# Kernel tuning notes

Hardware: AMD Instinct MI355X
Metric: run time of the kernel (lower is better)

Reference implementation:

```python
import jax, jax.numpy as jnp
import numpy as np

B, V, NB, K = 4, 5023, 10, 9
# (Cin, Cout) per NLayer: encoder Linear(3->16) then 3 encoder NLayers, 3 decoder NLayers, Linear(3->3)
CH = [(16, 16), (16, 16), (16, 32), (32, 16), (16, 16), (16, 3)]


def _glorot(key, shape):
    fan_in, fan_out = shape[0], shape[-1]
    s = np.float32(np.sqrt(2.0 / (fan_in + fan_out)))
    return (jax.random.normal(key, shape, dtype=jnp.float32) * s)


def setup_inputs():
    key = jax.random.key(0)
    ks = jax.random.split(key, 4 + 4 * len(CH))
    inp = {}
    inp["x"] = jax.random.normal(ks[0], (B, V, 3), dtype=jnp.float32)
    inp["adj"] = jax.random.randint(ks[1], (V, NB), 0, V + 1, dtype=jnp.int32)
    inp["Win"] = _glorot(ks[2], (3, CH[0][0]))
    inp["Wout"] = _glorot(ks[3], (CH[-1][1], 3))
    for i, (cin, cout) in enumerate(CH):
        k0, k1, k2, k3 = ks[4 + 4 * i], ks[5 + 4 * i], ks[6 + 4 * i], ks[7 + 4 * i]
        inp[f"W{i}"] = _glorot(k0, (cin, K, cout))
        inp[f"b{i}"] = jax.random.normal(k1, (cout,), dtype=jnp.float32) * 0.01
        inp[f"u{i}"] = _glorot(k2, (cin, K))
        inp[f"c{i}"] = jax.random.normal(k3, (K,), dtype=jnp.float32) * 0.01
    return inp


def _pad_gather(t, adj):
    # t: [B, V, ...]; pad a zero row at vertex index 0, gather neighbor features.
    z = jnp.zeros(t.shape[:1] + (1,) + t.shape[2:], t.dtype)
    return jnp.take(jnp.concatenate([z, t], axis=1), adj, axis=1)  # [B, V, NB, ...]


def _nlayer(h, adj, recip, W, b, u, c):
    # h: [B, V, Cin], W: [Cin, K, Cout], u: [Cin, K]
    wx = jnp.einsum('bvc,cko->bvko', h, W)          # [B, V, K, Cout]
    nb_w = _pad_gather(wx, adj)                      # [B, V, NB, K, Cout]
    ux = jnp.einsum('bvc,ck->bvk', h, u)             # [B, V, K]  (u and v maps share self.u)
    nb_u = _pad_gather(ux, adj)                      # [B, V, NB, K]
    q = jax.nn.softmax(ux[:, :, None, :] + nb_u + c, axis=-1)  # softmax over kernel dim
    out = jnp.einsum('bvnk,bvnko->bvo', q, nb_w)     # sum over neighbors & kernels
    return out * recip[None, :, None] + b


def reference(x, adj, Win, Wout, W0, b0, u0, c0, W1, b1, u1, c1, W2, b2, u2, c2,
              W3, b3, u3, c3, W4, b4, u4, c4, W5, b5, u5, c5):
    cnt = jnp.sum(adj != 0, axis=-1).astype(jnp.float32)        # [V]
    recip = jnp.where(cnt > 0, 1.0 / jnp.maximum(cnt, 1.0), 0.0)
    h = jax.nn.relu(x @ Win)
    layers = [(W0, b0, u0, c0), (W1, b1, u1, c1), (W2, b2, u2, c2),
              (W3, b3, u3, c3), (W4, b4, u4, c4), (W5, b5, u5, c5)]
    for (W, b, u, c) in layers:
        h = jax.nn.relu(_nlayer(h, adj, recip, W, b, u, c))
    return h @ Wout
```

## Files before the change

### kernel.cpp

```cpp
#include <hip/hip_runtime.h>

#define NBK 10
#define KK  9

constexpr int Bv  = 4;
constexpr int Vv  = 5023;
constexpr int TOT = Bv * Vv;
constexpr int UXP = 12;

__device__ __forceinline__ float merge16(float* a, int t)
{
#pragma unroll
    for (int j = 0; j < 8; j++) {
        float send = (t & 8) ? a[j] : a[j + 8];
        float keep = (t & 8) ? a[j + 8] : a[j];
        a[j] = keep + __shfl_xor(send, 8, 16);
    }
#pragma unroll
    for (int j = 0; j < 4; j++) {
        float send = (t & 4) ? a[j] : a[j + 4];
        float keep = (t & 4) ? a[j + 4] : a[j];
        a[j] = keep + __shfl_xor(send, 4, 16);
    }
#pragma unroll
    for (int j = 0; j < 2; j++) {
        float send = (t & 2) ? a[j] : a[j + 2];
        float keep = (t & 2) ? a[j + 2] : a[j];
        a[j] = keep + __shfl_xor(send, 2, 16);
    }
    {
        float send = (t & 1) ? a[0] : a[1];
        float keep = (t & 1) ? a[1] : a[0];
        a[0] = keep + __shfl_xor(send, 1, 16);
    }
    return a[0];
}

__global__ __launch_bounds__(256) void enc_l0_kernel(
    const float* __restrict__ x,
    const int*   __restrict__ adj,
    const float* __restrict__ Win,
    const float* __restrict__ u0,
    const float* __restrict__ W,
    const float* __restrict__ bvec,
    const float* __restrict__ cvec,
    const float* __restrict__ unx,
    float* __restrict__ hout,
    float* __restrict__ uxout)
{
    const int tid = threadIdx.x;
    const int g = tid >> 4;
    const int t = tid & 15;
    const int vv = blockIdx.x * 16 + g;
    if (vv >= TOT) return;
    const int b = vv / Vv;
    const int v = vv - b * Vv;
    const float* xB = x + (size_t)b * Vv * 3;

    int nb[NBK];
    const int2* arow = reinterpret_cast<const int2*>(&adj[v * NBK]);
#pragma unroll
    for (int j = 0; j < 5; j++) { int2 p = arow[j]; nb[2 * j] = p.x; nb[2 * j + 1] = p.y; }
    int cnt = 0;
#pragma unroll
    for (int n = 0; n < NBK; n++) cnt += (nb[n] != 0) ? 1 : 0;
    const float rec = cnt ? (1.0f / (float)cnt) : 0.0f;

    const float w0 = Win[t], w1 = Win[16 + t], w2 = Win[32 + t];
    float hn0[NBK];
#pragma unroll
    for (int n = 0; n < NBK; n++) {
        const int a = nb[n];
        float x0 = 0.f, x1 = 0.f, x2 = 0.f;
        if (a) {
            const float* xr = &xB[(size_t)(a - 1) * 3];
            x0 = xr[0]; x1 = xr[1]; x2 = xr[2];
        }
        hn0[n] = fmaxf(x0 * w0 + x1 * w1 + x2 * w2, 0.0f);
    }

    float q[KK] = {};
    if (t < NBK) {
        const float* xo = &xB[(size_t)v * 3];
        const float xo0 = xo[0], xo1 = xo[1], xo2 = xo[2];
        const int a = nb[t];
        float xn0 = 0.f, xn1 = 0.f, xn2 = 0.f;
        if (a) {
            const float* xr = &xB[(size_t)(a - 1) * 3];
            xn0 = xr[0]; xn1 = xr[1]; xn2 = xr[2];
        }
        float hs[16];
#pragma unroll
        for (int c = 0; c < 16; c++) {
            const float ho = fmaxf(xo0 * Win[c] + xo1 * Win[16 + c] + xo2 * Win[32 + c], 0.0f);
            const float hn = fmaxf(xn0 * Win[c] + xn1 * Win[16 + c] + xn2 * Win[32 + c], 0.0f);
            hs[c] = ho + hn;
        }
        float lg[KK];
#pragma unroll
        for (int k = 0; k < KK; k++) {
            float s = cvec[k];
#pragma unroll
            for (int c = 0; c < 16; c++) s = fmaf(hs[c], u0[c * KK + k], s);
            lg[k] = s;
        }
        float m = lg[0];
#pragma unroll
        for (int k = 1; k < KK; k++) m = fmaxf(m, lg[k]);
        float sum = 0.0f;
#pragma unroll
        for (int k = 0; k < KK; k++) { q[k] = __expf(lg[k] - m); sum += q[k]; }
        const float r = 1.0f / sum;
#pragma unroll
        for (int k = 0; k < KK; k++) q[k] *= r;
    }

    float g0[KK];
#pragma unroll
    for (int k = 0; k < KK; k++) g0[k] = 0.0f;
#pragma unroll
    for (int n = 0; n < NBK; n++) {
#pragma unroll
        for (int k = 0; k < KK; k++) {
            const float qnk = __shfl(q[k], n, 16);
            g0[k] = fmaf(qnk, hn0[n], g0[k]);
        }
    }

    float acc[16] = {};
#pragma unroll
    for (int k = 0; k < KK; k++) {
        const float4* wr = reinterpret_cast<const float4*>(&W[((size_t)t * KK + k) * 16]);
#pragma unroll
        for (int o4 = 0; o4 < 4; o4++) {
            const float4 w = wr[o4];
            acc[4 * o4 + 0] = fmaf(g0[k], w.x, acc[4 * o4 + 0]);
            acc[4 * o4 + 1] = fmaf(g0[k], w.y, acc[4 * o4 + 1]);
            acc[4 * o4 + 2] = fmaf(g0[k], w.z, acc[4 * o4 + 2]);
            acc[4 * o4 + 3] = fmaf(g0[k], w.w, acc[4 * o4 + 3]);
        }
    }

    const float o0 = merge16(acc, t);
    const float h0v = fmaxf(fmaf(o0, rec, bvec[t]), 0.0f);
    hout[(size_t)vv * 16 + t] = h0v;

    float uxv = 0.0f;
#pragma unroll
    for (int o = 0; o < 16; o++) {
        const float hb = __shfl(h0v, o, 16);
        if (t < KK) uxv = fmaf(hb, unx[o * KK + t], uxv);
    }
    if (t < KK) uxout[(size_t)vv * UXP + t] = uxv;
}

template<int CIN, int COUT, bool LAST>
__global__ __launch_bounds__(256) void nlayer_kernel(
    const float* __restrict__ hin,
    const float* __restrict__ uxin,
    const int*   __restrict__ adj,
    const float* __restrict__ W,
    const float* __restrict__ bvec,
    const float* __restrict__ cvec,
    const float* __restrict__ unx,
    float* __restrict__ hout,
    float* __restrict__ uxout,
    float* __restrict__ dout)
{
    constexpr int COUTP = (COUT == 32) ? 36 : ((COUT == 16) ? 20 : 4);

    __shared__ __align__(16) float s_w[KK * CIN * COUTP];
    __shared__ __align__(16) float s_q[16][NBK][12];

    const int tid = threadIdx.x;

    for (int i = tid; i < CIN * KK * COUT; i += 256) {
        const int c   = i / (KK * COUT);
        const int rem = i - c * (KK * COUT);
        const int k   = rem / COUT;
        const int o   = rem - k * COUT;
        s_w[(k * CIN + c) * COUTP + o] = W[i];
    }
    __syncthreads();

    const int g = tid >> 4;
    const int t = tid & 15;
    const int vv = blockIdx.x * 16 + g;
    if (vv >= TOT) return;
    const int b = vv / Vv;
    const int v = vv - b * Vv;
    const float* hinB  = hin  + (size_t)b * Vv * CIN;
    const float* uxinB = uxin + (size_t)b * Vv * UXP;

    int nb[NBK];
    const int2* arow = reinterpret_cast<const int2*>(&adj[v * NBK]);
#pragma unroll
    for (int j = 0; j < 5; j++) { int2 p = arow[j]; nb[2 * j] = p.x; nb[2 * j + 1] = p.y; }
    int cnt = 0;
#pragma unroll
    for (int n = 0; n < NBK; n++) cnt += (nb[n] != 0) ? 1 : 0;
    const float rec = cnt ? (1.0f / (float)cnt) : 0.0f;

    float hn0[NBK], hn1[NBK];
#pragma unroll
    for (int n = 0; n < NBK; n++) {
        const int a = nb[n];
        const float* hr = &hinB[(size_t)(a - 1) * CIN];
        hn0[n] = a ? hr[t] : 0.0f;
        if constexpr (CIN == 32) hn1[n] = a ? hr[t + 16] : 0.0f;
        else                     hn1[n] = 0.0f;
    }

    if (t < NBK) {
        const float* su = &uxinB[(size_t)v * UXP];
        const float4 s0 = *reinterpret_cast<const float4*>(su);
        const float4 s1 = *reinterpret_cast<const float4*>(su + 4);
        const float  s8 = su[8];
        const int a = nb[t];
        float4 n0 = make_float4(0.f, 0.f, 0.f, 0.f), n1 = n0;
        float  n8 = 0.0f;
        if (a) {
            const float* nu = &uxinB[(size_t)(a - 1) * UXP];
            n0 = *reinterpret_cast<const float4*>(nu);
            n1 = *reinterpret_cast<const float4*>(nu + 4);
            n8 = nu[8];
        }
        float lg[KK] = { s0.x + n0.x + cvec[0], s0.y + n0.y + cvec[1],
                         s0.z + n0.z + cvec[2], s0.w + n0.w + cvec[3],
                         s1.x + n1.x + cvec[4], s1.y + n1.y + cvec[5],
                         s1.z + n1.z + cvec[6], s1.w + n1.w + cvec[7],
                         s8 + n8 + cvec[8] };
        float m = lg[0];
#pragma unroll
        for (int k = 1; k < KK; k++) m = fmaxf(m, lg[k]);
        float e[KK], sum = 0.0f;
#pragma unroll
        for (int k = 0; k < KK; k++) { e[k] = __expf(lg[k] - m); sum += e[k]; }
        const float r = 1.0f / sum;
        *reinterpret_cast<float4*>(&s_q[g][t][0]) =
            make_float4(e[0] * r, e[1] * r, e[2] * r, e[3] * r);
        *reinterpret_cast<float4*>(&s_q[g][t][4]) =
            make_float4(e[4] * r, e[5] * r, e[6] * r, e[7] * r);
        s_q[g][t][8] = e[8] * r;
    }

    float g0[KK], g1[KK];
#pragma unroll
    for (int k = 0; k < KK; k++) { g0[k] = 0.0f; g1[k] = 0.0f; }
#pragma unroll
    for (int n = 0; n < NBK; n++) {
        const float4 qa = *reinterpret_cast<const float4*>(&s_q[g][n][0]);
        const float4 qb = *reinterpret_cast<const float4*>(&s_q[g][n][4]);
        const float  q8 = s_q[g][n][8];
        const float h0 = hn0[n];
        g0[0] = fmaf(qa.x, h0, g0[0]); g0[1] = fmaf(qa.y, h0, g0[1]);
        g0[2] = fmaf(qa.z, h0, g0[2]); g0[3] = fmaf(qa.w, h0, g0[3]);
        g0[4] = fmaf(qb.x, h0, g0[4]); g0[5] = fmaf(qb.y, h0, g0[5]);
        g0[6] = fmaf(qb.z, h0, g0[6]); g0[7] = fmaf(qb.w, h0, g0[7]);
        g0[8] = fmaf(q8,   h0, g0[8]);
        if constexpr (CIN == 32) {
            const float h1 = hn1[n];
            g1[0] = fmaf(qa.x, h1, g1[0]); g1[1] = fmaf(qa.y, h1, g1[1]);
            g1[2] = fmaf(qa.z, h1, g1[2]); g1[3] = fmaf(qa.w, h1, g1[3]);
            g1[4] = fmaf(qb.x, h1, g1[4]); g1[5] = fmaf(qb.y, h1, g1[5]);
            g1[6] = fmaf(qb.z, h1, g1[6]); g1[7] = fmaf(qb.w, h1, g1[7]);
            g1[8] = fmaf(q8,   h1, g1[8]);
        }
    }

    if constexpr (!LAST) {
        float acc[COUT] = {};
#pragma unroll
        for (int k = 0; k < KK; k++) {
            const float g0k = g0[k];
            const float* wr = &s_w[(k * CIN + t) * COUTP];
#pragma unroll
            for (int o4 = 0; o4 < COUT / 4; o4++) {
                const float4 w = *reinterpret_cast<const float4*>(&wr[4 * o4]);
                acc[4 * o4 + 0] = fmaf(g0k, w.x, acc[4 * o4 + 0]);
                acc[4 * o4 + 1] = fmaf(g0k, w.y, acc[4 * o4 + 1]);
                acc[4 * o4 + 2] = fmaf(g0k, w.z, acc[4 * o4 + 2]);
                acc[4 * o4 + 3] = fmaf(g0k, w.w, acc[4 * o4 + 3]);
            }
            if constexpr (CIN == 32) {
                const float g1k = g1[k];
                const float* wr2 = &s_w[(k * CIN + t + 16) * COUTP];
#pragma unroll
                for (int o4 = 0; o4 < COUT / 4; o4++) {
                    const float4 w = *reinterpret_cast<const float4*>(&wr2[4 * o4]);
                    acc[4 * o4 + 0] = fmaf(g1k, w.x, acc[4 * o4 + 0]);
                    acc[4 * o4 + 1] = fmaf(g1k, w.y, acc[4 * o4 + 1]);
                    acc[4 * o4 + 2] = fmaf(g1k, w.z, acc[4 * o4 + 2]);
                    acc[4 * o4 + 3] = fmaf(g1k, w.w, acc[4 * o4 + 3]);
                }
            }
        }

        const float o0 = merge16(acc, t);
        const float h0v = fmaxf(fmaf(o0, rec, bvec[t]), 0.0f);
        hout[(size_t)vv * COUT + t] = h0v;
        float h1v = 0.0f;
        if constexpr (COUT == 32) {
            const float o1 = merge16(acc + 16, t);
            h1v = fmaxf(fmaf(o1, rec, bvec[t + 16]), 0.0f);
            hout[(size_t)vv * COUT + 16 + t] = h1v;
        }

        float uxv = 0.0f;
#pragma unroll
        for (int o = 0; o < 16; o++) {
            const float hb = __shfl(h0v, o, 16);
            if (t < KK) uxv = fmaf(hb, unx[o * KK + t], uxv);
        }
        if constexpr (COUT == 32) {
#pragma unroll
            for (int o = 0; o < 16; o++) {
                const float hb = __shfl(h1v, o, 16);
                if (t < KK) uxv = fmaf(hb, unx[(o + 16) * KK + t], uxv);
            }
        }
        if (t < KK) uxout[(size_t)vv * UXP + t] = uxv;
    } else {
        float acc[3] = {};
#pragma unroll
        for (int k = 0; k < KK; k++) {
            const float4 w = *reinterpret_cast<const float4*>(&s_w[(k * CIN + t) * COUTP]);
            acc[0] = fmaf(g0[k], w.x, acc[0]);
            acc[1] = fmaf(g0[k], w.y, acc[1]);
            acc[2] = fmaf(g0[k], w.z, acc[2]);
        }
#pragma unroll
        for (int o = 0; o < 3; o++) {
            acc[o] += __shfl_xor(acc[o], 1, 16);
            acc[o] += __shfl_xor(acc[o], 2, 16);
            acc[o] += __shfl_xor(acc[o], 4, 16);
            acc[o] += __shfl_xor(acc[o], 8, 16);
        }
        float hnew[3];
#pragma unroll
        for (int o = 0; o < 3; o++)
            hnew[o] = fmaxf(fmaf(acc[o], rec, bvec[o]), 0.0f);
        if (t < 3) {
            float s = 0.0f;
#pragma unroll
            for (int j = 0; j < 3; j++)
                s = fmaf(hnew[j], unx[j * 3 + t], s);
            dout[(size_t)vv * 3 + t] = s;
        }
    }
}

extern "C" void kernel_launch(void* const* d_in, const int* in_sizes, int n_in,
                              void* d_out, int out_size, void* d_ws, size_t ws_size,
                              hipStream_t stream)
{
    const float* x    = (const float*)d_in[0];
    const int*   adj  = (const int*)  d_in[1];
    const float* Win  = (const float*)d_in[2];
    const float* Wout = (const float*)d_in[3];
    const float *W[6], *bb[6], *uu[6], *cc[6];
    for (int i = 0; i < 6; i++) {
        W[i]  = (const float*)d_in[4 + 4 * i];
        bb[i] = (const float*)d_in[5 + 4 * i];
        uu[i] = (const float*)d_in[6 + 4 * i];
        cc[i] = (const float*)d_in[7 + 4 * i];
    }
    float* out = (float*)d_out;

    float* p  = (float*)d_ws;
    float* h1 = p; p += (size_t)TOT * 16;
    float* h2 = p; p += (size_t)TOT * 16;
    float* h3 = p; p += (size_t)TOT * 32;
    float* h4 = p; p += (size_t)TOT * 16;
    float* h5 = p; p += (size_t)TOT * 16;
    float* u1 = p; p += (size_t)TOT * UXP;
    float* u2 = p; p += (size_t)TOT * UXP;
    float* u3 = p; p += (size_t)TOT * UXP;
    float* u4 = p; p += (size_t)TOT * UXP;
    float* u5 = p; p += (size_t)TOT * UXP;

    const int nb = (TOT + 15) / 16;

    enc_l0_kernel<<<nb, 256, 0, stream>>>(x, adj, Win, uu[0], W[0], bb[0], cc[0],
                                          uu[1], h1, u1);
    nlayer_kernel<16, 16, false><<<nb, 256, 0, stream>>>(h1, u1, adj, W[1], bb[1], cc[1], uu[2], h2, u2, nullptr);
    nlayer_kernel<16, 32, false><<<nb, 256, 0, stream>>>(h2, u2, adj, W[2], bb[2], cc[2], uu[3], h3, u3, nullptr);
    nlayer_kernel<32, 16, false><<<nb, 256, 0, stream>>>(h3, u3, adj, W[3], bb[3], cc[3], uu[4], h4, u4, nullptr);
    nlayer_kernel<16, 16, false><<<nb, 256, 0, stream>>>(h4, u4, adj, W[4], bb[4], cc[4], uu[5], h5, u5, nullptr);
    nlayer_kernel<16, 3, true ><<<nb, 256, 0, stream>>>(h5, u5, adj, W[5], bb[5], cc[5], Wout, nullptr, nullptr, out);
}
```

Baseline: 79.49 us.

## Interleave h and ux into one row buffer and overlap weight staging with gathers

Combines each layer's hidden features and ux projections into a single padded row per vertex (32 or 48 floats), so one neighbor gather touches one contiguous row instead of two separate buffers. The neighbor and ux loads are issued before the shared-memory weight staging and its barrier, so global gather latency overlaps the weight copy. The weight copy now uses float4 accesses, and layer 0 also stages its weights in shared memory instead of reading them from global memory. Out-of-range threads stay alive until the barrier, and the padded rows increase total bytes written.

```diff
diff --git a/kernel.cpp b/kernel.cpp
--- a/kernel.cpp
+++ b/kernel.cpp
@@ -6,7 +6,7 @@
 constexpr int Bv  = 4;
 constexpr int Vv  = 5023;
 constexpr int TOT = Bv * Vv;
-constexpr int UXP = 12;
+
 
 __device__ __forceinline__ float merge16(float* a, int t)
 {
@@ -45,55 +45,74 @@
     const float* __restrict__ bvec,
     const float* __restrict__ cvec,
     const float* __restrict__ unx,
-    float* __restrict__ hout,
-    float* __restrict__ uxout)
+    float* __restrict__ hux_out)
 {
+    constexpr int COUTP = 20;
+    __shared__ __align__(16) float s_w[KK * 16 * COUTP];
+
     const int tid = threadIdx.x;
     const int g = tid >> 4;
     const int t = tid & 15;
     const int vv = blockIdx.x * 16 + g;
-    if (vv >= TOT) return;
-    const int b = vv / Vv;
-    const int v = vv - b * Vv;
+    const bool act = vv < TOT;
+    int b = 0, v = 0;
+    if (act) { b = vv / Vv; v = vv - b * Vv; }
     const float* xB = x + (size_t)b * Vv * 3;
 
     int nb[NBK];
-    const int2* arow = reinterpret_cast<const int2*>(&adj[v * NBK]);
-#pragma unroll
-    for (int j = 0; j < 5; j++) { int2 p = arow[j]; nb[2 * j] = p.x; nb[2 * j + 1] = p.y; }
+    if (act) {
+        const int2* arow = reinterpret_cast<const int2*>(&adj[v * NBK]);
+#pragma unroll
+        for (int j = 0; j < 5; j++) { int2 p = arow[j]; nb[2 * j] = p.x; nb[2 * j + 1] = p.y; }
+    } else {
+#pragma unroll
+        for (int n = 0; n < NBK; n++) nb[n] = 0;
+    }
     int cnt = 0;
 #pragma unroll
     for (int n = 0; n < NBK; n++) cnt += (nb[n] != 0) ? 1 : 0;
     const float rec = cnt ? (1.0f / (float)cnt) : 0.0f;
 
+    float xn[NBK][3];
+#pragma unroll
+    for (int n = 0; n < NBK; n++) {
+        const int a = nb[n];
+        if (a) {
+            const float* xr = &xB[(size_t)(a - 1) * 3];
+            xn[n][0] = xr[0]; xn[n][1] = xr[1]; xn[n][2] = xr[2];
+        } else { xn[n][0] = 0.f; xn[n][1] = 0.f; xn[n][2] = 0.f; }
+    }
+    const float* xo = &xB[(size_t)v * 3];
+    const float xo0 = xo[0], xo1 = xo[1], xo2 = xo[2];
+
+    {
+        constexpr int NF4 = 16 * KK * 16 / 4;
+        constexpr int KC4 = KK * 16 / 4;
+        const float4* W4 = reinterpret_cast<const float4*>(W);
+        for (int i = tid; i < NF4; i += 256) {
+            const int c   = i / KC4;
+            const int rem = i - c * KC4;
+            const int k   = rem >> 2;
+            const int o4  = rem & 3;
+            *reinterpret_cast<float4*>(&s_w[(k * 16 + c) * COUTP + o4 * 4]) = W4[i];
+        }
+    }
+    __syncthreads();
+    if (!act) return;
+
     const float w0 = Win[t], w1 = Win[16 + t], w2 = Win[32 + t];
     float hn0[NBK];
 #pragma unroll
-    for (int n = 0; n < NBK; n++) {
-        const int a = nb[n];
-        float x0 = 0.f, x1 = 0.f, x2 = 0.f;
-        if (a) {
-            const float* xr = &xB[(size_t)(a - 1) * 3];
-            x0 = xr[0]; x1 = xr[1]; x2 = xr[2];
-        }
-        hn0[n] = fmaxf(x0 * w0 + x1 * w1 + x2 * w2, 0.0f);
-    }
+    for (int n = 0; n < NBK; n++)
+        hn0[n] = fmaxf(xn[n][0] * w0 + xn[n][1] * w1 + xn[n][2] * w2, 0.0f);
 
     float q[KK] = {};
     if (t < NBK) {
-        const float* xo = &xB[(size_t)v * 3];
-        const float xo0 = xo[0], xo1 = xo[1], xo2 = xo[2];
-        const int a = nb[t];
-        float xn0 = 0.f, xn1 = 0.f, xn2 = 0.f;
-        if (a) {
-            const float* xr = &xB[(size_t)(a - 1) * 3];
-            xn0 = xr[0]; xn1 = xr[1]; xn2 = xr[2];
-        }
         float hs[16];
 #pragma unroll
         for (int c = 0; c < 16; c++) {
             const float ho = fmaxf(xo0 * Win[c] + xo1 * Win[16 + c] + xo2 * Win[32 + c], 0.0f);
-            const float hn = fmaxf(xn0 * Win[c] + xn1 * Win[16 + c] + xn2 * Win[32 + c], 0.0f);
+            const float hn = fmaxf(xn[t][0] * Win[c] + xn[t][1] * Win[16 + c] + xn[t][2] * Win[32 + c], 0.0f);
             hs[c] = ho + hn;
         }
         float lg[KK];
@@ -130,20 +149,22 @@
     float acc[16] = {};
 #pragma unroll
     for (int k = 0; k < KK; k++) {
-        const float4* wr = reinterpret_cast<const float4*>(&W[((size_t)t * KK + k) * 16]);
+        const float g0k = g0[k];
+        const float* wr = &s_w[(k * 16 + t) * COUTP];
 #pragma unroll
         for (int o4 = 0; o4 < 4; o4++) {
-            const float4 w = wr[o4];
-            acc[4 * o4 + 0] = fmaf(g0[k], w.x, acc[4 * o4 + 0]);
-            acc[4 * o4 + 1] = fmaf(g0[k], w.y, acc[4 * o4 + 1]);
-            acc[4 * o4 + 2] = fmaf(g0[k], w.z, acc[4 * o4 + 2]);
-            acc[4 * o4 + 3] = fmaf(g0[k], w.w, acc[4 * o4 + 3]);
+            const float4 w = *reinterpret_cast<const float4*>(&wr[4 * o4]);
+            acc[4 * o4 + 0] = fmaf(g0k, w.x, acc[4 * o4 + 0]);
+            acc[4 * o4 + 1] = fmaf(g0k, w.y, acc[4 * o4 + 1]);
+            acc[4 * o4 + 2] = fmaf(g0k, w.z, acc[4 * o4 + 2]);
+            acc[4 * o4 + 3] = fmaf(g0k, w.w, acc[4 * o4 + 3]);
         }
     }
 
     const float o0 = merge16(acc, t);
     const float h0v = fmaxf(fmaf(o0, rec, bvec[t]), 0.0f);
-    hout[(size_t)vv * 16 + t] = h0v;
+    float* row = &hux_out[(size_t)vv * 32];
+    row[t] = h0v;
 
     float uxv = 0.0f;
 #pragma unroll
@@ -151,20 +172,18 @@
         const float hb = __shfl(h0v, o, 16);
         if (t < KK) uxv = fmaf(hb, unx[o * KK + t], uxv);
     }
-    if (t < KK) uxout[(size_t)vv * UXP + t] = uxv;
+    if (t < KK) row[16 + t] = uxv;
 }
 
-template<int CIN, int COUT, bool LAST>
+template<int CIN, int COUT, bool LAST, int RSI, int RSO>
 __global__ __launch_bounds__(256) void nlayer_kernel(
-    const float* __restrict__ hin,
-    const float* __restrict__ uxin,
+    const float* __restrict__ hux_in,
     const int*   __restrict__ adj,
     const float* __restrict__ W,
     const float* __restrict__ bvec,
     const float* __restrict__ cvec,
     const float* __restrict__ unx,
-    float* __restrict__ hout,
-    float* __restrict__ uxout,
+    float* __restrict__ hux_out,
     float* __restrict__ dout)
 {
     constexpr int COUTP = (COUT == 32) ? 36 : ((COUT == 16) ? 20 : 4);
@@ -173,29 +192,23 @@
     __shared__ __align__(16) float s_q[16][NBK][12];
 
     const int tid = threadIdx.x;
-
-    for (int i = tid; i < CIN * KK * COUT; i += 256) {
-        const int c   = i / (KK * COUT);
-        const int rem = i - c * (KK * COUT);
-        const int k   = rem / COUT;
-        const int o   = rem - k * COUT;
-        s_w[(k * CIN + c) * COUTP + o] = W[i];
-    }
-    __syncthreads();
-
     const int g = tid >> 4;
     const int t = tid & 15;
     const int vv = blockIdx.x * 16 + g;
-    if (vv >= TOT) return;
-    const int b = vv / Vv;
-    const int v = vv - b * Vv;
-    const float* hinB  = hin  + (size_t)b * Vv * CIN;
-    const float* uxinB = uxin + (size_t)b * Vv * UXP;
+    const bool act = vv < TOT;
+    int b = 0, v = 0;
+    if (act) { b = vv / Vv; v = vv - b * Vv; }
+    const float* inB = hux_in + (size_t)b * Vv * RSI;
 
     int nb[NBK];
-    const int2* arow = reinterpret_cast<const int2*>(&adj[v * NBK]);
-#pragma unroll
-    for (int j = 0; j < 5; j++) { int2 p = arow[j]; nb[2 * j] = p.x; nb[2 * j + 1] = p.y; }
+    if (act) {
+        const int2* arow = reinterpret_cast<const int2*>(&adj[v * NBK]);
+#pragma unroll
+        for (int j = 0; j < 5; j++) { int2 p = arow[j]; nb[2 * j] = p.x; nb[2 * j + 1] = p.y; }
+    } else {
+#pragma unroll
+        for (int n = 0; n < NBK; n++) nb[n] = 0;
+    }
     int cnt = 0;
 #pragma unroll
     for (int n = 0; n < NBK; n++) cnt += (nb[n] != 0) ? 1 : 0;
@@ -205,26 +218,53 @@
 #pragma unroll
     for (int n = 0; n < NBK; n++) {
         const int a = nb[n];
-        const float* hr = &hinB[(size_t)(a - 1) * CIN];
-        hn0[n] = a ? hr[t] : 0.0f;
-        if constexpr (CIN == 32) hn1[n] = a ? hr[t + 16] : 0.0f;
+        const float* r = &inB[(size_t)(a - 1) * RSI];
+        hn0[n] = a ? r[t] : 0.0f;
+        if constexpr (CIN == 32) hn1[n] = a ? r[t + 16] : 0.0f;
         else                     hn1[n] = 0.0f;
     }
 
+    float4 s0 = make_float4(0.f, 0.f, 0.f, 0.f), s1 = s0, n0 = s0, n1 = s0;
+    float  s8 = 0.f, n8 = 0.f;
     if (t < NBK) {
-        const float* su = &uxinB[(size_t)v * UXP];
-        const float4 s0 = *reinterpret_cast<const float4*>(su);
-        const float4 s1 = *reinterpret_cast<const float4*>(su + 4);
-        const float  s8 = su[8];
+        const float* su = &inB[(size_t)v * RSI + CIN];
+        s0 = *reinterpret_cast<const float4*>(su);
+        s1 = *reinterpret_cast<const float4*>(su + 4);
+        s8 = su[8];
         const int a = nb[t];
-        float4 n0 = make_float4(0.f, 0.f, 0.f, 0.f), n1 = n0;
-        float  n8 = 0.0f;
         if (a) {
-            const float* nu = &uxinB[(size_t)(a - 1) * UXP];
+            const float* nu = &inB[(size_t)(a - 1) * RSI + CIN];
             n0 = *reinterpret_cast<const float4*>(nu);
             n1 = *reinterpret_cast<const float4*>(nu + 4);
             n8 = nu[8];
         }
+    }
+
+    if constexpr (!LAST) {
+        constexpr int NF4 = CIN * KK * COUT / 4;
+        constexpr int KC4 = KK * COUT / 4;
+        constexpr int C4  = COUT / 4;
+        const float4* W4 = reinterpret_cast<const float4*>(W);
+        for (int i = tid; i < NF4; i += 256) {
+            const int c   = i / KC4;
+            const int rem = i - c * KC4;
+            const int k   = rem / C4;
+            const int o4  = rem - k * C4;
+            *reinterpret_cast<float4*>(&s_w[(k * CIN + c) * COUTP + o4 * 4]) = W4[i];
+        }
+    } else {
+        for (int i = tid; i < CIN * KK * 3; i += 256) {
+            const int c   = i / (KK * 3);
+            const int rem = i - c * (KK * 3);
+            const int k   = rem / 3;
+            const int o   = rem - k * 3;
+            s_w[(k * CIN + c) * COUTP + o] = W[i];
+        }
+    }
+    __syncthreads();
+    if (!act) return;
+
+    if (t < NBK) {
         float lg[KK] = { s0.x + n0.x + cvec[0], s0.y + n0.y + cvec[1],
                          s0.z + n0.z + cvec[2], s0.w + n0.w + cvec[3],
                          s1.x + n1.x + cvec[4], s1.y + n1.y + cvec[5],
@@ -298,12 +338,13 @@
 
         const float o0 = merge16(acc, t);
         const float h0v = fmaxf(fmaf(o0, rec, bvec[t]), 0.0f);
-        hout[(size_t)vv * COUT + t] = h0v;
+        float* row = &hux_out[(size_t)vv * RSO];
+        row[t] = h0v;
         float h1v = 0.0f;
         if constexpr (COUT == 32) {
             const float o1 = merge16(acc + 16, t);
             h1v = fmaxf(fmaf(o1, rec, bvec[t + 16]), 0.0f);
-            hout[(size_t)vv * COUT + 16 + t] = h1v;
+            row[16 + t] = h1v;
         }
 
         float uxv = 0.0f;
@@ -319,7 +360,7 @@
                 if (t < KK) uxv = fmaf(hb, unx[(o + 16) * KK + t], uxv);
             }
         }
-        if (t < KK) uxout[(size_t)vv * UXP + t] = uxv;
+        if (t < KK) row[COUT + t] = uxv;
     } else {
         float acc[3] = {};
 #pragma unroll
@@ -368,24 +409,19 @@
     float* out = (float*)d_out;
 
     float* p  = (float*)d_ws;
-    float* h1 = p; p += (size_t)TOT * 16;
-    float* h2 = p; p += (size_t)TOT * 16;
-    float* h3 = p; p += (size_t)TOT * 32;
-    float* h4 = p; p += (size_t)TOT * 16;
-    float* h5 = p; p += (size_t)TOT * 16;
-    float* u1 = p; p += (size_t)TOT * UXP;
-    float* u2 = p; p += (size_t)TOT * UXP;
-    float* u3 = p; p += (size_t)TOT * UXP;
-    float* u4 = p; p += (size_t)TOT * UXP;
-    float* u5 = p; p += (size_t)TOT * UXP;
+    float* B1 = p; p += (size_t)TOT * 32;
+    float* B2 = p; p += (size_t)TOT * 32;
+    float* B3 = p; p += (size_t)TOT * 48;
+    float* B4 = p; p += (size_t)TOT * 32;
+    float* B5 = p; p += (size_t)TOT * 32;
 
     const int nb = (TOT + 15) / 16;
 
     enc_l0_kernel<<<nb, 256, 0, stream>>>(x, adj, Win, uu[0], W[0], bb[0], cc[0],
-                                          uu[1], h1, u1);
-    nlayer_kernel<16, 16, false><<<nb, 256, 0, stream>>>(h1, u1, adj, W[1], bb[1], cc[1], uu[2], h2, u2, nullptr);
-    nlayer_kernel<16, 32, false><<<nb, 256, 0, stream>>>(h2, u2, adj, W[2], bb[2], cc[2], uu[3], h3, u3, nullptr);
-    nlayer_kernel<32, 16, false><<<nb, 256, 0, stream>>>(h3, u3, adj, W[3], bb[3], cc[3], uu[4], h4, u4, nullptr);
-    nlayer_kernel<16, 16, false><<<nb, 256, 0, stream>>>(h4, u4, adj, W[4], bb[4], cc[4], uu[5], h5, u5, nullptr);
-    nlayer_kernel<16, 3, true ><<<nb, 256, 0, stream>>>(h5, u5, adj, W[5], bb[5], cc[5], Wout, nullptr, nullptr, out);
+                                          uu[1], B1);
+    nlayer_kernel<16, 16, false, 32, 32><<<nb, 256, 0, stream>>>(B1, adj, W[1], bb[1], cc[1], uu[2], B2, nullptr);
+    nlayer_kernel<16, 32, false, 32, 48><<<nb, 256, 0, stream>>>(B2, adj, W[2], bb[2], cc[2], uu[3], B3, nullptr);
+    nlayer_kernel<32, 16, false, 48, 32><<<nb, 256, 0, stream>>>(B3, adj, W[3], bb[3], cc[3], uu[4], B4, nullptr);
+    nlayer_kernel<16, 16, false, 32, 32><<<nb, 256, 0, stream>>>(B4, adj, W[4], bb[4], cc[4], uu[5], B5, nullptr);
+    nlayer_kernel<16, 3, true, 32, 32><<<nb, 256, 0, stream>>>(B5, adj, W[5], bb[5], cc[5], Wout, nullptr, out);
 }
```

New measurement: 108.4 us. +36.3%, slower.
